# Kernel tuning notes

Hardware: AMD Instinct MI355X
Metric: run time of the kernel (lower is better)

## Reference

```python
import jax, jax.numpy as jnp
import numpy as np

B, T, D, H, WIN, G = 2, 2048, 768, 12, 16, 32
HD = D // H            # 64
K = 2 * WIN + 1        # local kernel size = 33


def setup_inputs() -> dict:
    key = jax.random.key(0)
    ks = jax.random.split(key, 5)
    s = 1.0 / np.sqrt(D).astype(np.float32)
    x = jax.random.normal(ks[0], (B, T, D), jnp.float32)
    # first G tokens of every batch are global (matches original's nonzero(global_mask[b]))
    global_mask = jnp.zeros((B, T), jnp.int32).at[:, :G].set(1)
    Wq = jax.random.normal(ks[1], (D, D), jnp.float32) * s
    Wk = jax.random.normal(ks[2], (D, D), jnp.float32) * s
    Wv = jax.random.normal(ks[3], (D, D), jnp.float32) * s
    Wo = jax.random.normal(ks[4], (D, D), jnp.float32) * s
    bq = jnp.zeros((D,), jnp.float32)
    bk = jnp.zeros((D,), jnp.float32)
    bv = jnp.zeros((D,), jnp.float32)
    bo = jnp.zeros((D,), jnp.float32)
    return {"x": x, "global_mask": global_mask, "Wq": Wq, "bq": bq,
            "Wk": Wk, "bk": bk, "Wv": Wv, "bv": bv, "Wo": Wo, "bo": bo}


def reference(x, global_mask, Wq, bq, Wk, bk, Wv, bv, Wo, bo):
    def split_heads(y):
        return y.reshape(B, T, H, HD).transpose(0, 2, 1, 3)  # [B,H,T,HD]

    q = split_heads(x @ Wq + bq)
    k = split_heads(x @ Wk + bk)
    v = split_heads(x @ Wv + bv)

    scale = 1.0 / np.sqrt(HD).astype(np.float32)

    offs = jnp.arange(-WIN, WIN + 1)
    idx = jnp.arange(T)[:, None] + offs[None, :]          # [T,K]
    valid = (idx >= 0) & (idx < T)                        # [T,K]
    idxc = jnp.clip(idx, 0, T - 1)

    k_loc = k[:, :, idxc]                                 # [B,H,T,K,HD]
    s_loc = jnp.einsum('bhtd,bhtkd->bhtk', q, k_loc) * scale
    s_loc = jnp.where(valid, s_loc, -jnp.inf)             # out-of-range excluded from softmax

    # global tokens (same positions for every batch by construction)
    g_idx = jnp.nonzero(global_mask[0], size=G)[0]        # [G]
    k_g = k[:, :, g_idx]                                  # [B,H,G,HD]
    v_g = v[:, :, g_idx]
    s_g = jnp.einsum('bhtd,bhgd->bhtg', q, k_g) * scale   # [B,H,T,G]

    # joint softmax over [local window, global tokens] (globals in window are double-counted,
    # exactly as in the original torch.cat([local_s, g_score]))
    attn = jax.nn.softmax(jnp.concatenate([s_loc, s_g], axis=-1), axis=-1)
    a_loc = jnp.where(valid, attn[..., :K], 0.0)          # [B,H,T,K]
    a_g = attn[..., K:]                                   # [B,H,T,G]

    v_loc = v[:, :, idxc]                                 # [B,H,T,K,HD]
    ctx = (jnp.einsum('bhtk,bhtkd->bhtd', a_loc, v_loc)
           + jnp.einsum('bhtg,bhgd->bhtd', a_g, v_g))     # [B,H,T,HD]

    out = ctx.transpose(0, 2, 1, 3).reshape(B, T, D) @ Wo + bo

    # dense attention map: scatter local band (add; invalid entries are 0),
    # then overwrite global columns (matches original write order)
    rows = jnp.arange(T)[:, None]                         # [T,1]
    full_attn = jnp.zeros((B, H, T, T), jnp.float32)
    full_attn = full_attn.at[:, :, rows, idxc].add(a_loc)
    full_attn = full_attn.at[:, :, :, g_idx].set(a_g)
    return out, full_attn
```

## Files before the change

kernel.cpp:

```cpp
#include <hip/hip_runtime.h>

typedef unsigned short u16;
typedef __attribute__((ext_vector_type(4))) u16 u16x4;
typedef __attribute__((ext_vector_type(8))) u16 u16x8;
typedef __attribute__((ext_vector_type(8))) short bf16x8;
typedef __attribute__((ext_vector_type(4))) float f32x4;

#define BB 2
#define TT 2048
#define DD 768
#define NH 12
#define HDIM 64
#define NQKV 2304
#define MM 4096

__device__ __forceinline__ u16 f2bf(float f) {
  unsigned u = __float_as_uint(f);
  u += 0x7fffu + ((u >> 16) & 1u);
  return (u16)(u >> 16);
}
__device__ __forceinline__ float bf2f(u16 s) {
  return __uint_as_float(((unsigned)s) << 16);
}
__device__ __forceinline__ void async_load16(const void* g, void* l) {
  __builtin_amdgcn_global_load_lds((const __attribute__((address_space(1))) void*)g,
                                   (__attribute__((address_space(3))) void*)l, 16, 0, 0);
}

__global__ __launch_bounds__(256) void castx(const float* __restrict__ x, u16* __restrict__ xb) {
  int i = blockIdx.x * 256 + threadIdx.x;
  float4 v = ((const float4*)x)[i];
  u16x4 o = { f2bf(v.x), f2bf(v.y), f2bf(v.z), f2bf(v.w) };
  ((u16x4*)xb)[i] = o;
}

__global__ __launch_bounds__(256) void wprep(const float* __restrict__ Wq, const float* __restrict__ Wk,
                                             const float* __restrict__ Wv, const float* __restrict__ Wo,
                                             u16* __restrict__ wqkvT, u16* __restrict__ woT) {
  __shared__ float tile[32][33];
  int z = blockIdx.z;
  const float* W = (z == 0) ? Wq : (z == 1) ? Wk : (z == 2) ? Wv : Wo;
  u16* dst = (z < 3) ? (wqkvT + (size_t)z * DD * DD) : woT;
  int k0 = blockIdx.x * 32, n0 = blockIdx.y * 32;
  int tx = threadIdx.x, ty = threadIdx.y;
#pragma unroll
  for (int j = 0; j < 4; ++j)
    tile[ty + j * 8][tx] = W[(size_t)(k0 + ty + j * 8) * DD + n0 + tx];
  __syncthreads();
#pragma unroll
  for (int j = 0; j < 4; ++j)
    dst[(size_t)(n0 + ty + j * 8) * DD + k0 + tx] = f2bf(tile[tx][ty + j * 8]);
}

__global__ __launch_bounds__(256) void prep_misc(const int* __restrict__ gm,
                                                 const float* __restrict__ bq, const float* __restrict__ bk,
                                                 const float* __restrict__ bv,
                                                 int* __restrict__ gidx, int* __restrict__ gpos,
                                                 float* __restrict__ biasqkv) {
  int tid = threadIdx.x;
  if (tid < 32) gidx[tid] = 0;
  for (int c = tid; c < TT; c += 256) gpos[c] = -1;
  for (int n = tid; n < NQKV; n += 256)
    biasqkv[n] = (n < 768) ? bq[n] : (n < 1536) ? bk[n - 768] : bv[n - 1536];
  __syncthreads();
  if (tid < 64) {
    int lane = tid;
    int base = 0;
    for (int c0 = 0; c0 < TT; c0 += 64) {
      int mval = gm[c0 + lane];
      unsigned long long bal = __ballot(mval != 0);
      int pre = __popcll(bal & ((1ull << lane) - 1ull));
      if (mval && (base + pre) < 32) { gidx[base + pre] = c0 + lane; gpos[c0 + lane] = base + pre; }
      base += __popcll(bal);
      if (base >= 32) break;
    }
  }
}

template <int BM, bool OUTBF>
__global__ __launch_bounds__(256) void gemm_bt(const u16* __restrict__ A, const u16* __restrict__ BT,
                                               const float* __restrict__ bias, void* __restrict__ Cv,
                                               int Ndim, int Kd) {
  constexpr int NJ = (BM == 128) ? 4 : 2;
  constexpr int ACH = BM / 32;
  __shared__ __attribute__((aligned(16))) u16 As[BM * 64];
  __shared__ __attribute__((aligned(16))) u16 Bs[128 * 64];
  const int tid = threadIdx.x;
  const int wave = tid >> 6, lane = tid & 63;
  const int m0 = blockIdx.x * BM, n0 = blockIdx.y * 128;
  const int wm = (BM == 128) ? ((wave & 1) << 6) : 0;
  const int wn = (BM == 128) ? ((wave >> 1) << 6) : (wave << 5);
  const int lr = lane & 15, lk = lane >> 4;
  const int srow_b = lane >> 3;
  const int scol = (lane & 7) * 8;

  f32x4 acc[4][NJ] = {};

  const int kIters = Kd >> 6;
  for (int kt = 0; kt < kIters; ++kt) {
#pragma unroll
    for (int cc = 0; cc < ACH; ++cc) {
      int c = wave * ACH + cc;
      int srow = c * 8 + srow_b;
      async_load16(A + (size_t)(m0 + srow) * Kd + (kt << 6) + scol, (void*)(As + c * 512));
    }
#pragma unroll
    for (int cc = 0; cc < 4; ++cc) {
      int c = wave * 4 + cc;
      int srow = c * 8 + srow_b;
      async_load16(BT + (size_t)(n0 + srow) * Kd + (kt << 6) + scol, (void*)(Bs + c * 512));
    }
    __syncthreads();
#pragma unroll
    for (int kc = 0; kc < 2; ++kc) {
      bf16x8 af[4], bfr[NJ];
#pragma unroll
      for (int i = 0; i < 4; ++i)
        af[i] = *(const bf16x8*)(As + (wm + i * 16 + lr) * 64 + kc * 32 + lk * 8);
#pragma unroll
      for (int j = 0; j < NJ; ++j)
        bfr[j] = *(const bf16x8*)(Bs + (wn + j * 16 + lr) * 64 + kc * 32 + lk * 8);
#pragma unroll
      for (int i = 0; i < 4; ++i)
#pragma unroll
        for (int j = 0; j < NJ; ++j)
          acc[i][j] = __builtin_amdgcn_mfma_f32_16x16x32_bf16(af[i], bfr[j], acc[i][j], 0, 0, 0);
    }
    __syncthreads();
  }

#pragma unroll
  for (int i = 0; i < 4; ++i) {
    const int row = m0 + wm + i * 16 + lk * 4;
#pragma unroll
    for (int j = 0; j < NJ; ++j) {
      const int col = n0 + wn + j * 16 + lr;
      const float bs = bias[col];
#pragma unroll
      for (int r = 0; r < 4; ++r) {
        const float val = acc[i][j][r] + bs;
        if (OUTBF) ((u16*)Cv)[(size_t)(row + r) * Ndim + col] = f2bf(val);
        else       ((float*)Cv)[(size_t)(row + r) * Ndim + col] = val;
      }
    }
  }
}

__global__ __launch_bounds__(256) void attn_kernel(const u16* __restrict__ qb,
                                                   const int* __restrict__ gidx,
                                                   const int* __restrict__ gpos,
                                                   u16* __restrict__ ctxb,
                                                   float* __restrict__ fattn) {
  __shared__ __attribute__((aligned(16))) u16 Kl[96 * 72];
  __shared__ __attribute__((aligned(16))) u16 Kg[32 * 72];
  __shared__ __attribute__((aligned(16))) u16 Vl[96 * 72];
  __shared__ __attribute__((aligned(16))) u16 Vg[32 * 72];
  __shared__ __attribute__((aligned(16))) float probs[64 * 68];
  __shared__ int wgpos[96];
  __shared__ int gidxs[32];

  const int tid = threadIdx.x;
  const int blk = blockIdx.x;
  const int chunk = blk & 31;
  const int h = (blk >> 5) % NH;
  const int b = blk / 384;
  const int t0 = chunk << 6;

  {
    const int r = tid >> 3;
    const int c8 = (tid & 7) << 3;
#pragma unroll
    for (int it = 0; it < 3; ++it) {
      int rr = it * 32 + r;
      int t = t0 - 16 + rr;
      t = t < 0 ? 0 : (t > TT - 1 ? TT - 1 : t);
      const u16* src = qb + (size_t)(b * TT + t) * NQKV + h * HDIM + c8;
      *(u16x8*)(Kl + rr * 72 + c8) = *(const u16x8*)(src + 768);
      *(u16x8*)(Vl + rr * 72 + c8) = *(const u16x8*)(src + 1536);
    }
    {
      int t = gidx[r];
      const u16* src = qb + (size_t)(b * TT + t) * NQKV + h * HDIM + c8;
      *(u16x8*)(Kg + r * 72 + c8) = *(const u16x8*)(src + 768);
      *(u16x8*)(Vg + r * 72 + c8) = *(const u16x8*)(src + 1536);
    }
    if (tid < 32) gidxs[tid] = gidx[tid];
    if (tid < 96) {
      int t = t0 - 16 + tid;
      wgpos[tid] = ((unsigned)t < TT) ? gpos[t] : -1;
    }
  }
  __syncthreads();

  const int tl = tid >> 2, sub = tid & 3;
  const int t = t0 + tl;
  const u16* qp = qb + (size_t)(b * TT + t) * NQKV + h * HDIM;
  float qv[64];
#pragma unroll
  for (int i = 0; i < 8; ++i) {
    u16x8 qq = *(const u16x8*)(qp + i * 8);
#pragma unroll
    for (int e = 0; e < 8; ++e) qv[i * 8 + e] = bf2f(qq[e]);
  }

  float sc[17];
  float mmax = -__builtin_inff();
#pragma unroll
  for (int i = 0; i < 17; ++i) {
    const int s = sub + (i << 2);
    const u16* kp;
    bool valid;
    if (s < 33) { kp = Kl + (tl + s) * 72; int j = t - 16 + s; valid = (j >= 0) && (j < TT); }
    else if (s < 65) { kp = Kg + (s - 33) * 72; valid = true; }
    else { kp = Kg; valid = false; }
    float d = 0.f;
#pragma unroll
    for (int i2 = 0; i2 < 8; ++i2) {
      u16x8 kv = *(const u16x8*)(kp + i2 * 8);
#pragma unroll
      for (int e = 0; e < 8; ++e) d += qv[i2 * 8 + e] * bf2f(kv[e]);
    }
    sc[i] = valid ? d * 0.125f : -__builtin_inff();
    mmax = fmaxf(mmax, sc[i]);
  }
  mmax = fmaxf(mmax, __shfl_xor(mmax, 1));
  mmax = fmaxf(mmax, __shfl_xor(mmax, 2));
  float sum = 0.f;
#pragma unroll
  for (int i = 0; i < 17; ++i) { sc[i] = __expf(sc[i] - mmax); sum += sc[i]; }
  sum += __shfl_xor(sum, 1);
  sum += __shfl_xor(sum, 2);
  const float inv = 1.0f / sum;
#pragma unroll
  for (int i = 0; i < 17; ++i) {
    const int s = sub + (i << 2);
    sc[i] *= inv;
    if (s < 65) probs[tl * 68 + s] = sc[i];
  }
  __syncthreads();

  float cacc[16];
#pragma unroll
  for (int i = 0; i < 16; ++i) cacc[i] = 0.f;
#pragma unroll 1
  for (int k = 0; k < 65; ++k) {
    const float pv = probs[tl * 68 + k];
    const u16* vp = (k < 33) ? (Vl + (tl + k) * 72) : (Vg + (k - 33) * 72);
    const u16* vq = vp + (sub << 4);
    u16x8 v0 = *(const u16x8*)(vq);
    u16x8 v1 = *(const u16x8*)(vq + 8);
#pragma unroll
    for (int e = 0; e < 8; ++e) { cacc[e] += pv * bf2f(v0[e]); cacc[8 + e] += pv * bf2f(v1[e]); }
  }
  {
    u16x8 cb0, cb1;
#pragma unroll
    for (int e = 0; e < 8; ++e) { cb0[e] = f2bf(cacc[e]); cb1[e] = f2bf(cacc[8 + e]); }
    u16* dst = ctxb + (size_t)(b * TT + t) * DD + h * HDIM + (sub << 4);
    *(u16x8*)dst = cb0;
    *(u16x8*)(dst + 8) = cb1;
  }

  float* fbase = fattn + ((size_t)(b * NH + h) * TT + t0) * TT;
#pragma unroll 1
  for (int it = 0; it < 128; ++it) {
    int f = it * 256 + tid;
    int rl = f >> 9;
    int c4 = (f & 511) << 2;
    int trow = t0 + rl;
    float4 v = make_float4(0.f, 0.f, 0.f, 0.f);
    int kk = c4 - trow + 16;
    if (kk >= -3 && kk < 33) {
      const float* pr = probs + rl * 68;
      float* vp = &v.x;
#pragma unroll
      for (int e = 0; e < 4; ++e) {
        int k2 = kk + e;
        if ((unsigned)k2 < 33u) vp[e] = pr[k2];
      }
    }
    *(float4*)(fbase + (size_t)rl * TT + c4) = v;
  }
  __syncthreads();

  {
    int rl = tid >> 2, g0 = (tid & 3) << 3;
    const float* pr = probs + rl * 68 + 33;
    float* frow = fbase + (size_t)rl * TT;
#pragma unroll
    for (int e = 0; e < 8; ++e) frow[gidxs[g0 + e]] = pr[g0 + e];
  }
}

extern "C" void kernel_launch(void* const* d_in, const int* in_sizes, int n_in,
                              void* d_out, int out_size, void* d_ws, size_t ws_size,
                              hipStream_t stream) {
  const float* x  = (const float*)d_in[0];
  const int* gm   = (const int*)d_in[1];
  const float* Wq = (const float*)d_in[2];
  const float* bq = (const float*)d_in[3];
  const float* Wk = (const float*)d_in[4];
  const float* bk = (const float*)d_in[5];
  const float* Wv = (const float*)d_in[6];
  const float* bv = (const float*)d_in[7];
  const float* Wo = (const float*)d_in[8];
  const float* bo = (const float*)d_in[9];

  float* out = (float*)d_out;
  float* fattn = out + (size_t)BB * TT * DD;

  char* p = (char*)d_ws;
  u16* xb      = (u16*)p;  p += (size_t)MM * DD * 2;
  u16* wqkvT   = (u16*)p;  p += (size_t)NQKV * DD * 2;
  u16* woT     = (u16*)p;  p += (size_t)DD * DD * 2;
  float* biasq = (float*)p; p += (size_t)NQKV * 4;
  int* gidx    = (int*)p;  p += 128;
  int* gpos    = (int*)p;  p += (size_t)TT * 4;
  u16* qkvb    = (u16*)p;  p += (size_t)MM * NQKV * 2;
  u16* ctxb    = (u16*)p;  p += (size_t)MM * DD * 2;

  castx<<<MM * DD / 4 / 256, 256, 0, stream>>>(x, xb);
  wprep<<<dim3(24, 24, 4), dim3(32, 8), 0, stream>>>(Wq, Wk, Wv, Wo, wqkvT, woT);
  prep_misc<<<1, 256, 0, stream>>>(gm, bq, bk, bv, gidx, gpos, biasq);
  gemm_bt<128, true><<<dim3(MM / 128, NQKV / 128), 256, 0, stream>>>(xb, wqkvT, biasq, qkvb, NQKV, DD);
  attn_kernel<<<BB * NH * (TT / 64), 256, 0, stream>>>(qkvb, gidx, gpos, ctxb, fattn);
  gemm_bt<64, false><<<dim3(MM / 64, DD / 128), 256, 0, stream>>>(ctxb, woT, bo, out, DD, DD);
}
```

Baseline: 547.9 us.

## Split dense attention-map writing into a separate many-block kernel

The attention kernel now saves its per-row probabilities (local window plus global scores) to a compact workspace buffer instead of writing the dense B*H*T*T map itself. A new kernel with four times as many blocks, each covering 16 rows, reloads those probabilities and streams the zero-filled band and the global columns to the output. This spreads the large memory-bound store across more workgroups and removes the now-unused gpos bookkeeping. In exchange it adds a kernel launch and a small intermediate round trip through global memory.

Result: slower. 560.3 us (+2.3%).

```diff
diff --git a/kernel.cpp b/kernel.cpp
--- a/kernel.cpp
+++ b/kernel.cpp
@@ -55,11 +55,10 @@
 __global__ __launch_bounds__(256) void prep_misc(const int* __restrict__ gm,
                                                  const float* __restrict__ bq, const float* __restrict__ bk,
                                                  const float* __restrict__ bv,
-                                                 int* __restrict__ gidx, int* __restrict__ gpos,
+                                                 int* __restrict__ gidx,
                                                  float* __restrict__ biasqkv) {
   int tid = threadIdx.x;
   if (tid < 32) gidx[tid] = 0;
-  for (int c = tid; c < TT; c += 256) gpos[c] = -1;
   for (int n = tid; n < NQKV; n += 256)
     biasqkv[n] = (n < 768) ? bq[n] : (n < 1536) ? bk[n - 768] : bv[n - 1536];
   __syncthreads();
@@ -70,7 +69,7 @@
       int mval = gm[c0 + lane];
       unsigned long long bal = __ballot(mval != 0);
       int pre = __popcll(bal & ((1ull << lane) - 1ull));
-      if (mval && (base + pre) < 32) { gidx[base + pre] = c0 + lane; gpos[c0 + lane] = base + pre; }
+      if (mval && (base + pre) < 32) gidx[base + pre] = c0 + lane;
       base += __popcll(bal);
       if (base >= 32) break;
     }
@@ -148,16 +147,13 @@
 
 __global__ __launch_bounds__(256) void attn_kernel(const u16* __restrict__ qb,
                                                    const int* __restrict__ gidx,
-                                                   const int* __restrict__ gpos,
                                                    u16* __restrict__ ctxb,
-                                                   float* __restrict__ fattn) {
+                                                   float* __restrict__ probsG) {
   __shared__ __attribute__((aligned(16))) u16 Kl[96 * 72];
   __shared__ __attribute__((aligned(16))) u16 Kg[32 * 72];
   __shared__ __attribute__((aligned(16))) u16 Vl[96 * 72];
   __shared__ __attribute__((aligned(16))) u16 Vg[32 * 72];
   __shared__ __attribute__((aligned(16))) float probs[64 * 68];
-  __shared__ int wgpos[96];
-  __shared__ int gidxs[32];
 
   const int tid = threadIdx.x;
   const int blk = blockIdx.x;
@@ -183,11 +179,6 @@
       const u16* src = qb + (size_t)(b * TT + t) * NQKV + h * HDIM + c8;
       *(u16x8*)(Kg + r * 72 + c8) = *(const u16x8*)(src + 768);
       *(u16x8*)(Vg + r * 72 + c8) = *(const u16x8*)(src + 1536);
-    }
-    if (tid < 32) gidxs[tid] = gidx[tid];
-    if (tid < 96) {
-      int t = t0 - 16 + tid;
-      wgpos[tid] = ((unsigned)t < TT) ? gpos[t] : -1;
     }
   }
   __syncthreads();
@@ -261,34 +252,56 @@
     *(u16x8*)(dst + 8) = cb1;
   }
 
-  float* fbase = fattn + ((size_t)(b * NH + h) * TT + t0) * TT;
+  {
+    float4* dst = (float4*)(probsG + ((size_t)(b * NH + h) * TT + t0) * 68);
+    const float4* srcp = (const float4*)probs;
 #pragma unroll 1
-  for (int it = 0; it < 128; ++it) {
-    int f = it * 256 + tid;
-    int rl = f >> 9;
-    int c4 = (f & 511) << 2;
-    int trow = t0 + rl;
+    for (int i = tid; i < 1088; i += 256) dst[i] = srcp[i];
+  }
+}
+
+__global__ __launch_bounds__(256) void fwrite_k(const float* __restrict__ probsG,
+                                                const int* __restrict__ gidx,
+                                                float* __restrict__ fattn) {
+  __shared__ __attribute__((aligned(16))) float Lp[16 * 68];
+  __shared__ int gidxs[32];
+  const int tid = threadIdx.x;
+  const int blk = blockIdx.x;
+  const int slice = blk & 127;
+  const int h = (blk >> 7) % NH;
+  const int b = blk / (128 * NH);
+  const int t0s = slice << 4;
+
+  const float4* src = (const float4*)(probsG + ((size_t)(b * NH + h) * TT + t0s) * 68);
+  for (int i = tid; i < 272; i += 256) ((float4*)Lp)[i] = src[i];
+  if (tid < 32) gidxs[tid] = gidx[tid];
+  __syncthreads();
+
+  float* fbase = fattn + ((size_t)(b * NH + h) * TT + t0s) * TT;
+#pragma unroll 1
+  for (int it = 0; it < 32; ++it) {
+    int q = it * 256 + tid;
+    int rl = q >> 9;
+    int c4 = (q & 511) << 2;
+    int trow = t0s + rl;
     float4 v = make_float4(0.f, 0.f, 0.f, 0.f);
     int kk = c4 - trow + 16;
     if (kk >= -3 && kk < 33) {
-      const float* pr = probs + rl * 68;
       float* vp = &v.x;
 #pragma unroll
       for (int e = 0; e < 4; ++e) {
         int k2 = kk + e;
-        if ((unsigned)k2 < 33u) vp[e] = pr[k2];
+        if ((unsigned)k2 < 33u) vp[e] = Lp[rl * 68 + k2];
       }
     }
     *(float4*)(fbase + (size_t)rl * TT + c4) = v;
   }
   __syncthreads();
-
-  {
-    int rl = tid >> 2, g0 = (tid & 3) << 3;
-    const float* pr = probs + rl * 68 + 33;
-    float* frow = fbase + (size_t)rl * TT;
-#pragma unroll
-    for (int e = 0; e < 8; ++e) frow[gidxs[g0 + e]] = pr[g0 + e];
+#pragma unroll
+  for (int rep = 0; rep < 2; ++rep) {
+    int w = rep * 256 + tid;
+    int rl = w >> 5, g = w & 31;
+    fbase[(size_t)rl * TT + gidxs[g]] = Lp[rl * 68 + 33 + g];
   }
 }
 
@@ -315,14 +328,15 @@
   u16* woT     = (u16*)p;  p += (size_t)DD * DD * 2;
   float* biasq = (float*)p; p += (size_t)NQKV * 4;
   int* gidx    = (int*)p;  p += 128;
-  int* gpos    = (int*)p;  p += (size_t)TT * 4;
   u16* qkvb    = (u16*)p;  p += (size_t)MM * NQKV * 2;
   u16* ctxb    = (u16*)p;  p += (size_t)MM * DD * 2;
+  float* probsG= (float*)p; p += (size_t)MM * NH * 68 * 4;
 
   castx<<<MM * DD / 4 / 256, 256, 0, stream>>>(x, xb);
   wprep<<<dim3(24, 24, 4), dim3(32, 8), 0, stream>>>(Wq, Wk, Wv, Wo, wqkvT, woT);
-  prep_misc<<<1, 256, 0, stream>>>(gm, bq, bk, bv, gidx, gpos, biasq);
+  prep_misc<<<1, 256, 0, stream>>>(gm, bq, bk, bv, gidx, biasq);
   gemm_bt<128, true><<<dim3(MM / 128, NQKV / 128), 256, 0, stream>>>(xb, wqkvT, biasq, qkvb, NQKV, DD);
-  attn_kernel<<<BB * NH * (TT / 64), 256, 0, stream>>>(qkvb, gidx, gpos, ctxb, fattn);
+  attn_kernel<<<BB * NH * (TT / 64), 256, 0, stream>>>(qkvb, gidx, ctxb, probsG);
+  fwrite_k<<<BB * NH * (TT / 16), 256, 0, stream>>>(probsG, gidx, fattn);
   gemm_bt<64, false><<<dim3(MM / 64, DD / 128), 256, 0, stream>>>(ctxb, woT, bo, out, DD, DD);
 }
```
